# Kernel optimization log

Hardware: AMD Instinct MI355X
Metric: run time of the kernel (lower is better)

The kernel has to match this reference:

```python
import jax, jax.numpy as jnp
import numpy as np

N_NODES = 100000
N_HYPEREDGES = 50000
N_CAND = 200000
SET_SIZE = 8
EMB_DIM = 64


def setup_inputs() -> dict:
    key = jax.random.key(0)
    k1, k2, k3, k4 = jax.random.split(key, 4)
    node_emb = jax.random.normal(k1, (N_NODES, EMB_DIM), dtype=jnp.float32)
    hyperedge_emb = jax.random.normal(k2, (N_HYPEREDGES, EMB_DIM), dtype=jnp.float32)
    h = jax.random.randint(k3, (N_CAND,), 0, N_HYPEREDGES, dtype=jnp.int64)
    X = jax.random.randint(k4, (N_CAND, SET_SIZE), 0, N_NODES, dtype=jnp.int64)
    return {"node_emb": node_emb, "hyperedge_emb": hyperedge_emb, "h": h, "X": X}


def reference(node_emb, hyperedge_emb, h, X):
    # Gather per-candidate embeddings
    src = hyperedge_emb[h]          # [E, d]
    embs = node_emb[X]              # [E, S, d]

    # star_: min over nodes of sigmoid(<hyperedge, node>)
    star_scores = jax.nn.sigmoid(jnp.einsum('ed,esd->es', src, embs))  # [E, S]
    star = jnp.min(star_scores, axis=1, keepdims=True)                 # [E, 1]

    # clique_: min over all pairs of sigmoid(<node_i, node_j>)
    pair_scores = jax.nn.sigmoid(jnp.einsum('esd,etd->est', embs, embs))  # [E, S, S]
    clique = jnp.min(pair_scores, axis=(1, 2), keepdims=False)[:, None]   # [E, 1]

    return jnp.concatenate([star, clique], axis=-1)  # [E, 2]
```

## Files before the change

kernel.cpp:

```cpp
#include <hip/hip_runtime.h>
#include <math.h>

#define SET_SIZE 8
#define EMB_DIM 64
#define NPAIR 36
#define NDOT (SET_SIZE + NPAIR)

__device__ __forceinline__ float dot4(float4 a, float4 b) {
    return fmaf(a.x, b.x, fmaf(a.y, b.y, fmaf(a.z, b.z, a.w * b.w)));
}

__global__ __launch_bounds__(256) void hyperedge_score_g8(
    const float* __restrict__ node_emb,
    const float* __restrict__ hyperedge_emb,
    const int*   __restrict__ h,
    const int*   __restrict__ X,
    float*       __restrict__ out,
    int n_cand)
{
    int tid = blockIdx.x * blockDim.x + threadIdx.x;
    int grp = tid >> 3;
    int q   = tid & 7;
    if (grp >= n_cand) return;

    const int4* Xv = (const int4*)(X + (size_t)grp * SET_SIZE);
    int4 x0 = Xv[0];
    int4 x1 = Xv[1];
    int he = h[grp];
    int idx[SET_SIZE] = {x0.x, x0.y, x0.z, x0.w, x1.x, x1.y, x1.z, x1.w};

    float4 va[9], vb[9];
#pragma unroll
    for (int r = 0; r < SET_SIZE; ++r) {
        const float4* p = (const float4*)(node_emb + (size_t)idx[r] * EMB_DIM) + 2 * q;
        va[r] = p[0];
        vb[r] = p[1];
    }
    {
        const float4* p = (const float4*)(hyperedge_emb + (size_t)he * EMB_DIM) + 2 * q;
        va[8] = p[0];
        vb[8] = p[1];
    }

    float acc[NDOT];
#pragma unroll
    for (int s = 0; s < SET_SIZE; ++s)
        acc[s] = dot4(va[8], va[s]) + dot4(vb[8], vb[s]);
    {
        int k = SET_SIZE;
#pragma unroll
        for (int s = 0; s < SET_SIZE; ++s) {
#pragma unroll
            for (int t = s; t < SET_SIZE; ++t, ++k)
                acc[k] = dot4(va[s], va[t]) + dot4(vb[s], vb[t]);
        }
    }

#pragma unroll
    for (int i = 0; i < NDOT; ++i) {
        float x = acc[i];
        x += __shfl_xor(x, 1);
        x += __shfl_xor(x, 2);
        x += __shfl_xor(x, 4);
        acc[i] = x;
    }

    float smin = acc[0];
#pragma unroll
    for (int s = 1; s < SET_SIZE; ++s) smin = fminf(smin, acc[s]);
    float pmin = acc[SET_SIZE];
#pragma unroll
    for (int i = 1; i < NPAIR; ++i) pmin = fminf(pmin, acc[SET_SIZE + i]);

    float res = (q == 0) ? 1.0f / (1.0f + __expf(-smin))
                         : 1.0f / (1.0f + __expf(-pmin));
    if (q < 2) out[(size_t)grp * 2 + q] = res;
}

extern "C" void kernel_launch(void* const* d_in, const int* in_sizes, int n_in,
                              void* d_out, int out_size, void* d_ws, size_t ws_size,
                              hipStream_t stream) {
    const float* node_emb      = (const float*)d_in[0];
    const float* hyperedge_emb = (const float*)d_in[1];
    const int*   h             = (const int*)d_in[2];
    const int*   X             = (const int*)d_in[3];
    float*       out           = (float*)d_out;

    int n_cand = in_sizes[2];

    int block = 256;
    long long total_threads = (long long)n_cand * 8;
    int grid = (int)((total_threads + block - 1) / block);
    hyperedge_score_g8<<<grid, block, 0, stream>>>(
        node_emb, hyperedge_emb, h, X, out, n_cand);
}
```

Baseline: 134.2 us.

## Convert embeddings to fp16 in workspace and score with packed fdot2

Adds pre-pass kernels that convert the node and hyperedge embedding tables to fp16 in workspace. The scoring kernel then gathers half as many bytes per row and computes dots with v_dot2 f16 instructions accumulating in fp32. The aim is to cut gather bandwidth in a memory-bound random-access kernel, at the cost of an extra full-table conversion pass each call and reduced input precision. If the workspace is too small, it falls back to the original fp32 kernel.

```diff
diff --git a/kernel.cpp b/kernel.cpp
--- a/kernel.cpp
+++ b/kernel.cpp
@@ -1,4 +1,5 @@
 #include <hip/hip_runtime.h>
+#include <hip/hip_fp16.h>
 #include <math.h>
 
 #define SET_SIZE 8
@@ -6,16 +7,50 @@
 #define NPAIR 36
 #define NDOT (SET_SIZE + NPAIR)
 
-__device__ __forceinline__ float dot4(float4 a, float4 b) {
-    return fmaf(a.x, b.x, fmaf(a.y, b.y, fmaf(a.z, b.z, a.w * b.w)));
-}
-
-__global__ __launch_bounds__(256) void hyperedge_score_g8(
-    const float* __restrict__ node_emb,
-    const float* __restrict__ hyperedge_emb,
-    const int*   __restrict__ h,
-    const int*   __restrict__ X,
-    float*       __restrict__ out,
+typedef _Float16 f16x2 __attribute__((ext_vector_type(2)));
+
+union Frag16 {
+    float4 f4;
+    f16x2  h2[4];
+};
+
+__device__ __forceinline__ float dot8_f16(const Frag16& a, const Frag16& b, float c) {
+#if __has_builtin(__builtin_amdgcn_fdot2)
+    c = __builtin_amdgcn_fdot2(a.h2[0], b.h2[0], c, false);
+    c = __builtin_amdgcn_fdot2(a.h2[1], b.h2[1], c, false);
+    c = __builtin_amdgcn_fdot2(a.h2[2], b.h2[2], c, false);
+    c = __builtin_amdgcn_fdot2(a.h2[3], b.h2[3], c, false);
+#else
+#pragma unroll
+    for (int j = 0; j < 4; ++j) {
+        c = fmaf((float)a.h2[j].x, (float)b.h2[j].x, c);
+        c = fmaf((float)a.h2[j].y, (float)b.h2[j].y, c);
+    }
+#endif
+    return c;
+}
+
+__global__ __launch_bounds__(256) void cvt_f32_f16_kernel(
+    const float* __restrict__ in, __half* __restrict__ out, int n8)
+{
+    int i = blockIdx.x * blockDim.x + threadIdx.x;
+    if (i >= n8) return;
+    const float4* p = (const float4*)in + 2 * (size_t)i;
+    float4 a = p[0], b = p[1];
+    union { __half2 h2[4]; float4 f4; } u;
+    u.h2[0] = __floats2half2_rn(a.x, a.y);
+    u.h2[1] = __floats2half2_rn(a.z, a.w);
+    u.h2[2] = __floats2half2_rn(b.x, b.y);
+    u.h2[3] = __floats2half2_rn(b.z, b.w);
+    ((float4*)out)[i] = u.f4;
+}
+
+__global__ __launch_bounds__(256) void hyperedge_score_f16(
+    const __half* __restrict__ node_f16,
+    const __half* __restrict__ he_f16,
+    const int*    __restrict__ h,
+    const int*    __restrict__ X,
+    float*        __restrict__ out,
     int n_cand)
 {
     int tid = blockIdx.x * blockDim.x + threadIdx.x;
@@ -29,30 +64,23 @@
     int he = h[grp];
     int idx[SET_SIZE] = {x0.x, x0.y, x0.z, x0.w, x1.x, x1.y, x1.z, x1.w};
 
-    float4 va[9], vb[9];
-#pragma unroll
-    for (int r = 0; r < SET_SIZE; ++r) {
-        const float4* p = (const float4*)(node_emb + (size_t)idx[r] * EMB_DIM) + 2 * q;
-        va[r] = p[0];
-        vb[r] = p[1];
-    }
-    {
-        const float4* p = (const float4*)(hyperedge_emb + (size_t)he * EMB_DIM) + 2 * q;
-        va[8] = p[0];
-        vb[8] = p[1];
-    }
+    Frag16 v[9];
+#pragma unroll
+    for (int r = 0; r < SET_SIZE; ++r)
+        v[r].f4 = *((const float4*)(node_f16 + (size_t)idx[r] * EMB_DIM) + q);
+    v[8].f4 = *((const float4*)(he_f16 + (size_t)he * EMB_DIM) + q);
 
     float acc[NDOT];
 #pragma unroll
     for (int s = 0; s < SET_SIZE; ++s)
-        acc[s] = dot4(va[8], va[s]) + dot4(vb[8], vb[s]);
+        acc[s] = dot8_f16(v[8], v[s], 0.0f);
     {
         int k = SET_SIZE;
 #pragma unroll
         for (int s = 0; s < SET_SIZE; ++s) {
 #pragma unroll
             for (int t = s; t < SET_SIZE; ++t, ++k)
-                acc[k] = dot4(va[s], va[t]) + dot4(vb[s], vb[t]);
+                acc[k] = dot8_f16(v[s], v[t], 0.0f);
         }
     }
 
@@ -72,6 +100,64 @@
 #pragma unroll
     for (int i = 1; i < NPAIR; ++i) pmin = fminf(pmin, acc[SET_SIZE + i]);
 
+    float res = (q == 0) ? 1.0f / (1.0f + __expf(-smin))
+                         : 1.0f / (1.0f + __expf(-pmin));
+    if (q < 2) out[(size_t)grp * 2 + q] = res;
+}
+
+__device__ __forceinline__ float dot4f(float4 a, float4 b) {
+    return fmaf(a.x, b.x, fmaf(a.y, b.y, fmaf(a.z, b.z, a.w * b.w)));
+}
+
+__global__ __launch_bounds__(256) void hyperedge_score_f32(
+    const float* __restrict__ node_emb, const float* __restrict__ hyperedge_emb,
+    const int* __restrict__ h, const int* __restrict__ X,
+    float* __restrict__ out, int n_cand)
+{
+    int tid = blockIdx.x * blockDim.x + threadIdx.x;
+    int grp = tid >> 3;
+    int q   = tid & 7;
+    if (grp >= n_cand) return;
+    const int4* Xv = (const int4*)(X + (size_t)grp * SET_SIZE);
+    int4 x0 = Xv[0]; int4 x1 = Xv[1];
+    int he = h[grp];
+    int idx[SET_SIZE] = {x0.x, x0.y, x0.z, x0.w, x1.x, x1.y, x1.z, x1.w};
+    float4 va[9], vb[9];
+#pragma unroll
+    for (int r = 0; r < SET_SIZE; ++r) {
+        const float4* p = (const float4*)(node_emb + (size_t)idx[r] * EMB_DIM) + 2 * q;
+        va[r] = p[0]; vb[r] = p[1];
+    }
+    {
+        const float4* p = (const float4*)(hyperedge_emb + (size_t)he * EMB_DIM) + 2 * q;
+        va[8] = p[0]; vb[8] = p[1];
+    }
+    float acc[NDOT];
+#pragma unroll
+    for (int s = 0; s < SET_SIZE; ++s)
+        acc[s] = dot4f(va[8], va[s]) + dot4f(vb[8], vb[s]);
+    {
+        int k = SET_SIZE;
+#pragma unroll
+        for (int s = 0; s < SET_SIZE; ++s)
+#pragma unroll
+            for (int t = s; t < SET_SIZE; ++t, ++k)
+                acc[k] = dot4f(va[s], va[t]) + dot4f(vb[s], vb[t]);
+    }
+#pragma unroll
+    for (int i = 0; i < NDOT; ++i) {
+        float x = acc[i];
+        x += __shfl_xor(x, 1);
+        x += __shfl_xor(x, 2);
+        x += __shfl_xor(x, 4);
+        acc[i] = x;
+    }
+    float smin = acc[0];
+#pragma unroll
+    for (int s = 1; s < SET_SIZE; ++s) smin = fminf(smin, acc[s]);
+    float pmin = acc[SET_SIZE];
+#pragma unroll
+    for (int i = 1; i < NPAIR; ++i) pmin = fminf(pmin, acc[SET_SIZE + i]);
     float res = (q == 0) ? 1.0f / (1.0f + __expf(-smin))
                          : 1.0f / (1.0f + __expf(-pmin));
     if (q < 2) out[(size_t)grp * 2 + q] = res;
@@ -86,11 +172,30 @@
     const int*   X             = (const int*)d_in[3];
     float*       out           = (float*)d_out;
 
-    int n_cand = in_sizes[2];
-
+    int n_node_elems = in_sizes[0];
+    int n_he_elems   = in_sizes[1];
+    int n_cand       = in_sizes[2];
+
+    size_t need = ((size_t)n_node_elems + (size_t)n_he_elems) * sizeof(__half);
     int block = 256;
     long long total_threads = (long long)n_cand * 8;
-    int grid = (int)((total_threads + block - 1) / block);
-    hyperedge_score_g8<<<grid, block, 0, stream>>>(
-        node_emb, hyperedge_emb, h, X, out, n_cand);
-}
+    int grid_main = (int)((total_threads + block - 1) / block);
+
+    if (ws_size >= need) {
+        __half* node_f16 = (__half*)d_ws;
+        __half* he_f16   = node_f16 + n_node_elems;
+
+        int n8_node = n_node_elems / 8;
+        int n8_he   = n_he_elems / 8;
+        cvt_f32_f16_kernel<<<(n8_node + block - 1) / block, block, 0, stream>>>(
+            node_emb, node_f16, n8_node);
+        cvt_f32_f16_kernel<<<(n8_he + block - 1) / block, block, 0, stream>>>(
+            hyperedge_emb, he_f16, n8_he);
+
+        hyperedge_score_f16<<<grid_main, block, 0, stream>>>(
+            node_f16, he_f16, h, X, out, n_cand);
+    } else {
+        hyperedge_score_f32<<<grid_main, block, 0, stream>>>(
+            node_emb, hyperedge_emb, h, X, out, n_cand);
+    }
+}
```

Result: faster. 125.6 us (-6.4%).
